# Kernel optimization log

Measured on AMD Instinct MI355X. Metric: run time of the kernel, lower is better.

## Reference

```python
import jax, jax.numpy as jnp
import numpy as np

N, E, IN_DIM, HID, L = 50000, 800000, 64, 64, 3
EDGE_DIM = 2 * HID + 2  # src_h | dst_h | edge_feat


def setup_inputs() -> dict:
    key = jax.random.key(0)
    ks = jax.random.split(key, 32)
    s = 0.05
    inp = {
        "h": jax.random.normal(ks[0], (N, IN_DIM), jnp.float32),
        "e": jax.random.normal(ks[1], (E, 2), jnp.float32),
        "src": jax.random.randint(ks[2], (E,), 0, N),
        "dst": jax.random.randint(ks[3], (E,), 0, N),
        # input embedding
        "emb_W": jax.random.normal(ks[4], (IN_DIM, HID), jnp.float32) * s,
        "emb_b": jnp.zeros((HID,), jnp.float32),
        # per-GIN-layer params (stacked over L)
        "eps": jnp.zeros((L,), jnp.float32),  # learn_eps init 0
        "mlp_W1": jax.random.normal(ks[5], (L, HID, HID), jnp.float32) * s,
        "mlp_b1": jnp.zeros((L, HID), jnp.float32),
        "mlp_bn_s": jnp.ones((L, HID), jnp.float32),   # eval-mode BN folded: x*s+sh
        "mlp_bn_sh": jnp.zeros((L, HID), jnp.float32),
        "mlp_W2": jax.random.normal(ks[6], (L, HID, HID), jnp.float32) * s,
        "mlp_b2": jnp.zeros((L, HID), jnp.float32),
        "apply_bn_s": jnp.ones((L, HID), jnp.float32),
        "apply_bn_sh": jnp.zeros((L, HID), jnp.float32),
        "gin_bn_s": jnp.ones((L, HID), jnp.float32),
        "gin_bn_sh": jnp.zeros((L, HID), jnp.float32),
        # prediction heads (L+1 of them)
        "pred_W1": jax.random.normal(ks[7], (L + 1, EDGE_DIM, HID), jnp.float32) * s,
        "pred_b1": jnp.zeros((L + 1, HID), jnp.float32),
        "pred_W2": jax.random.normal(ks[8], (L + 1, HID, 1), jnp.float32) * s,
        "pred_b2": jnp.zeros((L + 1, 1), jnp.float32),
    }
    return inp


def reference(h, e, src, dst, emb_W, emb_b, eps,
              mlp_W1, mlp_b1, mlp_bn_s, mlp_bn_sh, mlp_W2, mlp_b2,
              apply_bn_s, apply_bn_sh, gin_bn_s, gin_bn_sh,
              pred_W1, pred_b1, pred_W2, pred_b2):
    n = h.shape[0]
    bn = lambda x, sc, sh: x * sc + sh  # eval-mode batchnorm (folded scale/shift)

    h = h @ emb_W + emb_b  # [N, HID]

    def edge_feat(hh):
        # gather node features onto edges: [E, 2*HID+2]
        return jnp.concatenate([hh[src], hh[dst], e], axis=1)

    def pred(ef, i):
        z = jax.nn.relu(ef @ pred_W1[i] + pred_b1[i])
        return z @ pred_W2[i] + pred_b2[i]  # [E, 1]

    score = pred(edge_feat(h), 0)
    for i in range(L):
        h_in = h
        # GIN sum aggregation: copy src features, sum at dst
        neigh = jax.ops.segment_sum(h[src], dst, num_segments=n)
        x = (1.0 + eps[i]) * h + neigh
        # MLP: Linear -> BN -> ReLU -> Linear
        x = jax.nn.relu(bn(x @ mlp_W1[i] + mlp_b1[i], mlp_bn_s[i], mlp_bn_sh[i]))
        x = x @ mlp_W2[i] + mlp_b2[i]
        # ApplyNodeFunc: BN -> ReLU
        x = jax.nn.relu(bn(x, apply_bn_s[i], apply_bn_sh[i]))
        # GINLayer post: BN -> ReLU -> residual (dropout=0 in eval)
        x = jax.nn.relu(bn(x, gin_bn_s[i], gin_bn_sh[i]))
        h = h_in + x
        score = score + pred(edge_feat(h), i + 1)
    return jax.nn.relu(score)
```

## Files before the change

kernel.cpp:

```cpp
#include <hip/hip_runtime.h>
#include <hip/hip_bf16.h>

#define HID 64
#define L 3

typedef unsigned short ushort_t;
typedef unsigned int uint_t;

static __device__ __forceinline__ ushort_t f2bf(float f) {
    uint_t u = __float_as_uint(f);
    uint_t r = (u + 0x7FFFu + ((u >> 16) & 1u)) >> 16;
    return (ushort_t)r;
}
static __device__ __forceinline__ float bf2f(ushort_t u) {
    return __uint_as_float(((uint_t)u) << 16);
}

template <int OUT_BF16>
__global__ __launch_bounds__(256) void k_matmul16(
    const float* __restrict__ in, const float* __restrict__ W,
    const float* __restrict__ bias, void* __restrict__ out, int N)
{
    __shared__ float xs[16][68];
    const int row16 = threadIdx.x >> 4;
    const int li    = threadIdx.x & 15;
    const int r     = blockIdx.x * 16 + row16;
    if (r >= N) return;
    float4 x4 = *(const float4*)(in + (size_t)r * 64 + 4 * li);
    xs[row16][4*li+0] = x4.x; xs[row16][4*li+1] = x4.y;
    xs[row16][4*li+2] = x4.z; xs[row16][4*li+3] = x4.w;
    float4 acc;
    if (bias) acc = *(const float4*)(bias + 4 * li);
    else      acc = make_float4(0.f, 0.f, 0.f, 0.f);
#pragma unroll
    for (int k = 0; k < 64; k++) {
        float xk = xs[row16][k];
        float4 wv = *(const float4*)(W + k * 64 + 4 * li);
        acc.x += xk * wv.x; acc.y += xk * wv.y;
        acc.z += xk * wv.z; acc.w += xk * wv.w;
    }
    if (OUT_BF16) {
        ushort_t* op = (ushort_t*)out + (size_t)r * 64 + 4 * li;
        ushort4 o;
        o.x = f2bf(acc.x); o.y = f2bf(acc.y); o.z = f2bf(acc.z); o.w = f2bf(acc.w);
        *(ushort4*)op = o;
    } else {
        *(float4*)((float*)out + (size_t)r * 64 + 4 * li) = acc;
    }
}

__global__ __launch_bounds__(256) void k_gin_fused(
    const float* __restrict__ h, float* __restrict__ hout,
    const int* __restrict__ csr_src, const int* __restrict__ offsets,
    const float* __restrict__ epsp,
    const float* __restrict__ W1, const float* __restrict__ b1,
    const float* __restrict__ s1, const float* __restrict__ sh1,
    const float* __restrict__ W2, const float* __restrict__ b2,
    const float* __restrict__ as_, const float* __restrict__ ash,
    const float* __restrict__ gs, const float* __restrict__ gsh, int N)
{
    __shared__ float xs[16][68];
    __shared__ float ts[16][68];
    const int row16 = threadIdx.x >> 4;
    const int li    = threadIdx.x & 15;
    const int r     = blockIdx.x * 16 + row16;
    if (r >= N) return;

    int beg = offsets[r], end = offsets[r + 1];
    float4 acc = make_float4(0.f, 0.f, 0.f, 0.f);
    int k = beg;
    for (; k + 1 < end; k += 2) {
        int s0 = csr_src[k], s1i = csr_src[k + 1];
        float4 v0 = *(const float4*)(h + (size_t)s0 * 64 + 4 * li);
        float4 v1 = *(const float4*)(h + (size_t)s1i * 64 + 4 * li);
        acc.x += v0.x + v1.x; acc.y += v0.y + v1.y;
        acc.z += v0.z + v1.z; acc.w += v0.w + v1.w;
    }
    if (k < end) {
        int s0 = csr_src[k];
        float4 v0 = *(const float4*)(h + (size_t)s0 * 64 + 4 * li);
        acc.x += v0.x; acc.y += v0.y; acc.z += v0.z; acc.w += v0.w;
    }

    const float epsv = 1.0f + epsp[0];
    float4 hv = *(const float4*)(h + (size_t)r * 64 + 4 * li);
    xs[row16][4*li+0] = epsv * hv.x + acc.x;
    xs[row16][4*li+1] = epsv * hv.y + acc.y;
    xs[row16][4*li+2] = epsv * hv.z + acc.z;
    xs[row16][4*li+3] = epsv * hv.w + acc.w;

    float4 t = *(const float4*)(b1 + 4 * li);
#pragma unroll
    for (int kk = 0; kk < 64; kk++) {
        float xk = xs[row16][kk];
        float4 wv = *(const float4*)(W1 + kk * 64 + 4 * li);
        t.x += xk * wv.x; t.y += xk * wv.y; t.z += xk * wv.z; t.w += xk * wv.w;
    }
    {
        float4 sc = *(const float4*)(s1 + 4 * li);
        float4 sh = *(const float4*)(sh1 + 4 * li);
        t.x = t.x * sc.x + sh.x; t.x = t.x > 0.f ? t.x : 0.f;
        t.y = t.y * sc.y + sh.y; t.y = t.y > 0.f ? t.y : 0.f;
        t.z = t.z * sc.z + sh.z; t.z = t.z > 0.f ? t.z : 0.f;
        t.w = t.w * sc.w + sh.w; t.w = t.w > 0.f ? t.w : 0.f;
    }
    ts[row16][4*li+0] = t.x; ts[row16][4*li+1] = t.y;
    ts[row16][4*li+2] = t.z; ts[row16][4*li+3] = t.w;

    float4 u = *(const float4*)(b2 + 4 * li);
#pragma unroll
    for (int kk = 0; kk < 64; kk++) {
        float tk = ts[row16][kk];
        float4 wv = *(const float4*)(W2 + kk * 64 + 4 * li);
        u.x += tk * wv.x; u.y += tk * wv.y; u.z += tk * wv.z; u.w += tk * wv.w;
    }
    {
        float4 sc = *(const float4*)(as_ + 4 * li);
        float4 sh = *(const float4*)(ash + 4 * li);
        u.x = u.x * sc.x + sh.x; u.x = u.x > 0.f ? u.x : 0.f;
        u.y = u.y * sc.y + sh.y; u.y = u.y > 0.f ? u.y : 0.f;
        u.z = u.z * sc.z + sh.z; u.z = u.z > 0.f ? u.z : 0.f;
        u.w = u.w * sc.w + sh.w; u.w = u.w > 0.f ? u.w : 0.f;
        sc = *(const float4*)(gs + 4 * li);
        sh = *(const float4*)(gsh + 4 * li);
        u.x = u.x * sc.x + sh.x; u.x = u.x > 0.f ? u.x : 0.f;
        u.y = u.y * sc.y + sh.y; u.y = u.y > 0.f ? u.y : 0.f;
        u.z = u.z * sc.z + sh.z; u.z = u.z > 0.f ? u.z : 0.f;
        u.w = u.w * sc.w + sh.w; u.w = u.w > 0.f ? u.w : 0.f;
    }
    float4 o = make_float4(hv.x + u.x, hv.y + u.y, hv.z + u.z, hv.w + u.w);
    *(float4*)(hout + (size_t)r * 64 + 4 * li) = o;
}

__global__ __launch_bounds__(256) void k_count(
    const int* __restrict__ dst, int* __restrict__ deg, int E)
{
    int e = blockIdx.x * 256 + threadIdx.x;
    if (e < E) atomicAdd(&deg[dst[e]], 1);
}

__global__ __launch_bounds__(1024) void k_scan(
    int* __restrict__ cursor, int* __restrict__ offsets, int N)
{
    __shared__ int wsum[16];
    __shared__ int carry_s;
    int tid = threadIdx.x, lane = tid & 63, wid = tid >> 6;
    if (tid == 0) carry_s = 0;
    __syncthreads();
    for (int base = 0; base < N; base += 1024) {
        int idx = base + tid;
        int v = (idx < N) ? cursor[idx] : 0;
        int x = v;
#pragma unroll
        for (int o = 1; o < 64; o <<= 1) {
            int t = __shfl_up(x, o, 64);
            if (lane >= o) x += t;
        }
        if (lane == 63) wsum[wid] = x;
        __syncthreads();
        if (wid == 0) {
            int s = (lane < 16) ? wsum[lane] : 0;
#pragma unroll
            for (int o = 1; o < 16; o <<= 1) {
                int t = __shfl_up(s, o, 64);
                if (lane >= o) s += t;
            }
            if (lane < 16) wsum[lane] = s;
        }
        __syncthreads();
        int woff  = (wid > 0) ? wsum[wid - 1] : 0;
        int carry = carry_s;
        int total = wsum[15];
        int excl  = carry + woff + x - v;
        if (idx < N) { offsets[idx] = excl; cursor[idx] = excl; }
        __syncthreads();
        if (tid == 0) carry_s = carry + total;
        __syncthreads();
        if (tid == 0 && base + 1024 >= N) offsets[N] = carry + total;
    }
}

__global__ __launch_bounds__(256) void k_fill(
    const int* __restrict__ src, const int* __restrict__ dst,
    int* __restrict__ cursor, int* __restrict__ csr_src, int E)
{
    int e = blockIdx.x * 256 + threadIdx.x;
    if (e >= E) return;
    int pos = atomicAdd(&cursor[dst[e]], 1);
    csr_src[pos] = src[e];
}

template <int MODE>
__global__ __launch_bounds__(256, 4) void k_edge(
    const ushort_t* __restrict__ A, const ushort_t* __restrict__ Bm,
    const float* __restrict__ e,
    const int* __restrict__ src, const int* __restrict__ dst,
    const float* __restrict__ Wc,
    const float* __restrict__ W2,
    const float* __restrict__ b2p,
    float* __restrict__ score, int E)
{
    const int li = threadIdx.x & 15;
    const float4 wc0 = *(const float4*)(Wc + li*4);
    const float4 wc1 = *(const float4*)(Wc + 64 + li*4);
    const float4 w2  = *(const float4*)(W2 + li*4);
    const float b2 = b2p[0];
    int g  = (blockIdx.x * 256 + threadIdx.x) >> 4;
    int ng = (gridDim.x * 256) >> 4;
    for (int idx = g; idx < E; idx += ng) {
        int s = src[idx];
        int d = dst[idx];
        float2 ev = *(const float2*)(e + 2*(size_t)idx);
        ushort4 au = *(const ushort4*)(A  + (size_t)s*64 + li*4);
        ushort4 bu = *(const ushort4*)(Bm + (size_t)d*64 + li*4);
        float z0 = bf2f(au.x) + bf2f(bu.x) + ev.x*wc0.x + ev.y*wc1.x; z0 = z0 > 0.f ? z0 : 0.f;
        float z1 = bf2f(au.y) + bf2f(bu.y) + ev.x*wc0.y + ev.y*wc1.y; z1 = z1 > 0.f ? z1 : 0.f;
        float z2 = bf2f(au.z) + bf2f(bu.z) + ev.x*wc0.z + ev.y*wc1.z; z2 = z2 > 0.f ? z2 : 0.f;
        float z3 = bf2f(au.w) + bf2f(bu.w) + ev.x*wc0.w + ev.y*wc1.w; z3 = z3 > 0.f ? z3 : 0.f;
        float p = z0*w2.x + z1*w2.y + z2*w2.z + z3*w2.w;
        p += __shfl_xor(p, 1);
        p += __shfl_xor(p, 2);
        p += __shfl_xor(p, 4);
        p += __shfl_xor(p, 8);
        if (li == 0) {
            if (MODE == 0) {
                score[idx] = p + b2;
            } else if (MODE == 1) {
                score[idx] += p + b2;
            } else {
                float v = score[idx] + p + b2;
                score[idx] = v > 0.f ? v : 0.f;
            }
        }
    }
}

extern "C" void kernel_launch(void* const* d_in, const int* in_sizes, int n_in,
                              void* d_out, int out_size, void* d_ws, size_t ws_size,
                              hipStream_t stream) {
    const float* h_in  = (const float*)d_in[0];
    const float* e     = (const float*)d_in[1];
    const int*   src   = (const int*)d_in[2];
    const int*   dst   = (const int*)d_in[3];
    const float* emb_W = (const float*)d_in[4];
    const float* emb_b = (const float*)d_in[5];
    const float* eps   = (const float*)d_in[6];
    const float* mW1   = (const float*)d_in[7];
    const float* mb1   = (const float*)d_in[8];
    const float* mbs   = (const float*)d_in[9];
    const float* mbsh  = (const float*)d_in[10];
    const float* mW2   = (const float*)d_in[11];
    const float* mb2   = (const float*)d_in[12];
    const float* as_   = (const float*)d_in[13];
    const float* ash   = (const float*)d_in[14];
    const float* gs    = (const float*)d_in[15];
    const float* gsh   = (const float*)d_in[16];
    const float* pW1   = (const float*)d_in[17];
    const float* pb1   = (const float*)d_in[18];
    const float* pW2   = (const float*)d_in[19];
    const float* pb2   = (const float*)d_in[20];

    const int N = in_sizes[0] / 64;
    const int E = in_sizes[2];

    float* score = (float*)d_out;

    char* wp = (char*)d_ws;
    float* h0 = (float*)wp;         wp += (size_t)N * 64 * 4;
    float* h1 = (float*)wp;         wp += (size_t)N * 64 * 4;
    ushort_t* Abuf = (ushort_t*)wp; wp += (size_t)N * 64 * 2;
    ushort_t* Bbuf = (ushort_t*)wp; wp += (size_t)N * 64 * 2;
    int* offsets = (int*)wp;        wp += (size_t)(N + 1) * 4;
    int* cursor  = (int*)wp;        wp += (size_t)N * 4;
    int* csr_src = (int*)wp;

    const int rowBlocks = (N + 15) / 16;
    const int edgeGrid  = (E + 255) / 256;
    const int edgeBlocks = 2048;

    hipMemsetAsync(cursor, 0, (size_t)N * sizeof(int), stream);
    k_count<<<edgeGrid, 256, 0, stream>>>(dst, cursor, E);
    k_scan<<<1, 1024, 0, stream>>>(cursor, offsets, N);
    k_fill<<<edgeGrid, 256, 0, stream>>>(src, dst, cursor, csr_src, E);

    k_matmul16<0><<<rowBlocks, 256, 0, stream>>>(h_in, emb_W, emb_b, h0, N);

    float* hcur = h0;
    float* hnext = h1;

    for (int i = 0; i <= L; i++) {
        const float* pw = pW1 + (size_t)i * 130 * 64;
        k_matmul16<1><<<rowBlocks, 256, 0, stream>>>(hcur, pw,          pb1 + i*64, Abuf, N);
        k_matmul16<1><<<rowBlocks, 256, 0, stream>>>(hcur, pw + 64*64,  nullptr,    Bbuf, N);

        const float* Wc = pw + 128 * 64;
        const float* w2 = pW2 + (size_t)i * 64;
        const float* b2 = pb2 + i;
        if (i == 0) {
            k_edge<0><<<edgeBlocks, 256, 0, stream>>>(Abuf, Bbuf, e, src, dst,
                                                      Wc, w2, b2, score, E);
        } else if (i < L) {
            k_edge<1><<<edgeBlocks, 256, 0, stream>>>(Abuf, Bbuf, e, src, dst,
                                                      Wc, w2, b2, score, E);
        } else {
            k_edge<2><<<edgeBlocks, 256, 0, stream>>>(Abuf, Bbuf, e, src, dst,
                                                      Wc, w2, b2, score, E);
        }

        if (i < L) {
            k_gin_fused<<<rowBlocks, 256, 0, stream>>>(
                hcur, hnext, csr_src, offsets, eps + i,
                mW1 + (size_t)i*64*64, mb1 + i*64, mbs + i*64, mbsh + i*64,
                mW2 + (size_t)i*64*64, mb2 + i*64,
                as_ + i*64, ash + i*64, gs + i*64, gsh + i*64, N);
            float* tmp = hcur; hcur = hnext; hnext = tmp;
        }
    }
}
```

Baseline: 728.2 us.

## Fuse edge scoring into CSR-ordered GIN aggregation and merge A/B projections

Edge prediction now runs inside the per-destination GIN aggregation kernel. CSR entries carry (src, edge id), so the destination row of B is loaded once per node and the src gather for A shares the loop with aggregation. The two projection matmuls become one kernel that reads h once, and an optional bf16 copy of h halves the bytes of the neighbour gather. In exchange, score writes and edge-feature reads become scattered by edge id, work per thread follows the destination's degree, and aggregating in bf16 changes numerics.

```diff
diff --git a/kernel.cpp b/kernel.cpp
--- a/kernel.cpp
+++ b/kernel.cpp
@@ -16,10 +16,10 @@
     return __uint_as_float(((uint_t)u) << 16);
 }
 
-template <int OUT_BF16>
-__global__ __launch_bounds__(256) void k_matmul16(
+__global__ __launch_bounds__(256) void k_embed(
     const float* __restrict__ in, const float* __restrict__ W,
-    const float* __restrict__ bias, void* __restrict__ out, int N)
+    const float* __restrict__ bias, float* __restrict__ out,
+    ushort_t* __restrict__ outbf, int N)
 {
     __shared__ float xs[16][68];
     const int row16 = threadIdx.x >> 4;
@@ -29,9 +29,7 @@
     float4 x4 = *(const float4*)(in + (size_t)r * 64 + 4 * li);
     xs[row16][4*li+0] = x4.x; xs[row16][4*li+1] = x4.y;
     xs[row16][4*li+2] = x4.z; xs[row16][4*li+3] = x4.w;
-    float4 acc;
-    if (bias) acc = *(const float4*)(bias + 4 * li);
-    else      acc = make_float4(0.f, 0.f, 0.f, 0.f);
+    float4 acc = *(const float4*)(bias + 4 * li);
 #pragma unroll
     for (int k = 0; k < 64; k++) {
         float xk = xs[row16][k];
@@ -39,19 +37,113 @@
         acc.x += xk * wv.x; acc.y += xk * wv.y;
         acc.z += xk * wv.z; acc.w += xk * wv.w;
     }
-    if (OUT_BF16) {
-        ushort_t* op = (ushort_t*)out + (size_t)r * 64 + 4 * li;
+    *(float4*)(out + (size_t)r * 64 + 4 * li) = acc;
+    if (outbf) {
         ushort4 o;
         o.x = f2bf(acc.x); o.y = f2bf(acc.y); o.z = f2bf(acc.z); o.w = f2bf(acc.w);
-        *(ushort4*)op = o;
-    } else {
-        *(float4*)((float*)out + (size_t)r * 64 + 4 * li) = acc;
-    }
-}
-
-__global__ __launch_bounds__(256) void k_gin_fused(
+        *(ushort4*)(outbf + (size_t)r * 64 + 4 * li) = o;
+    }
+}
+
+__global__ __launch_bounds__(256) void k_matmulAB(
+    const float* __restrict__ h, const float* __restrict__ WA,
+    const float* __restrict__ bA, const float* __restrict__ WB,
+    ushort_t* __restrict__ A, ushort_t* __restrict__ B, int N)
+{
+    __shared__ float xs[16][68];
+    const int row16 = threadIdx.x >> 4;
+    const int li    = threadIdx.x & 15;
+    const int r     = blockIdx.x * 16 + row16;
+    if (r >= N) return;
+    float4 x4 = *(const float4*)(h + (size_t)r * 64 + 4 * li);
+    xs[row16][4*li+0] = x4.x; xs[row16][4*li+1] = x4.y;
+    xs[row16][4*li+2] = x4.z; xs[row16][4*li+3] = x4.w;
+    float4 accA = *(const float4*)(bA + 4 * li);
+    float4 accB = make_float4(0.f, 0.f, 0.f, 0.f);
+#pragma unroll
+    for (int k = 0; k < 64; k++) {
+        float xk = xs[row16][k];
+        float4 wa = *(const float4*)(WA + k * 64 + 4 * li);
+        float4 wb = *(const float4*)(WB + k * 64 + 4 * li);
+        accA.x += xk * wa.x; accA.y += xk * wa.y;
+        accA.z += xk * wa.z; accA.w += xk * wa.w;
+        accB.x += xk * wb.x; accB.y += xk * wb.y;
+        accB.z += xk * wb.z; accB.w += xk * wb.w;
+    }
+    ushort4 oa, ob;
+    oa.x = f2bf(accA.x); oa.y = f2bf(accA.y); oa.z = f2bf(accA.z); oa.w = f2bf(accA.w);
+    ob.x = f2bf(accB.x); ob.y = f2bf(accB.y); ob.z = f2bf(accB.z); ob.w = f2bf(accB.w);
+    *(ushort4*)(A + (size_t)r * 64 + 4 * li) = oa;
+    *(ushort4*)(B + (size_t)r * 64 + 4 * li) = ob;
+}
+
+__global__ __launch_bounds__(256) void k_count(
+    const int* __restrict__ dst, int* __restrict__ deg, int E)
+{
+    int e = blockIdx.x * 256 + threadIdx.x;
+    if (e < E) atomicAdd(&deg[dst[e]], 1);
+}
+
+__global__ __launch_bounds__(1024) void k_scan(
+    int* __restrict__ cursor, int* __restrict__ offsets, int N)
+{
+    __shared__ int wsum[16];
+    __shared__ int carry_s;
+    int tid = threadIdx.x, lane = tid & 63, wid = tid >> 6;
+    if (tid == 0) carry_s = 0;
+    __syncthreads();
+    for (int base = 0; base < N; base += 1024) {
+        int idx = base + tid;
+        int v = (idx < N) ? cursor[idx] : 0;
+        int x = v;
+#pragma unroll
+        for (int o = 1; o < 64; o <<= 1) {
+            int t = __shfl_up(x, o, 64);
+            if (lane >= o) x += t;
+        }
+        if (lane == 63) wsum[wid] = x;
+        __syncthreads();
+        if (wid == 0) {
+            int s = (lane < 16) ? wsum[lane] : 0;
+#pragma unroll
+            for (int o = 1; o < 16; o <<= 1) {
+                int t = __shfl_up(s, o, 64);
+                if (lane >= o) s += t;
+            }
+            if (lane < 16) wsum[lane] = s;
+        }
+        __syncthreads();
+        int woff  = (wid > 0) ? wsum[wid - 1] : 0;
+        int carry = carry_s;
+        int total = wsum[15];
+        int excl  = carry + woff + x - v;
+        if (idx < N) { offsets[idx] = excl; cursor[idx] = excl; }
+        __syncthreads();
+        if (tid == 0) carry_s = carry + total;
+        __syncthreads();
+        if (tid == 0 && base + 1024 >= N) offsets[N] = carry + total;
+    }
+}
+
+__global__ __launch_bounds__(256) void k_fill(
+    const int* __restrict__ src, const int* __restrict__ dst,
+    int* __restrict__ cursor, int2* __restrict__ csr_se, int E)
+{
+    int e = blockIdx.x * 256 + threadIdx.x;
+    if (e >= E) return;
+    int pos = atomicAdd(&cursor[dst[e]], 1);
+    csr_se[pos] = make_int2(src[e], e);
+}
+
+template <int MODE, int HASGIN, int AGGBF>
+__global__ __launch_bounds__(256) void k_fused(
     const float* __restrict__ h, float* __restrict__ hout,
-    const int* __restrict__ csr_src, const int* __restrict__ offsets,
+    const ushort_t* __restrict__ hbf, ushort_t* __restrict__ hbfout,
+    const ushort_t* __restrict__ A, const ushort_t* __restrict__ Bm,
+    const float* __restrict__ ep,
+    const int2* __restrict__ csr_se, const int* __restrict__ offsets,
+    const float* __restrict__ Wc, const float* __restrict__ W2v,
+    const float* __restrict__ b2p, float* __restrict__ score,
     const float* __restrict__ epsp,
     const float* __restrict__ W1, const float* __restrict__ b1,
     const float* __restrict__ s1, const float* __restrict__ sh1,
@@ -66,21 +158,102 @@
     const int r     = blockIdx.x * 16 + row16;
     if (r >= N) return;
 
+    const float4 wc0 = *(const float4*)(Wc + li*4);
+    const float4 wc1 = *(const float4*)(Wc + 64 + li*4);
+    const float4 w2v = *(const float4*)(W2v + li*4);
+    const float bb2 = b2p[0];
+    ushort4 bu = *(const ushort4*)(Bm + (size_t)r * 64 + li*4);
+    const float4 brow = make_float4(bf2f(bu.x), bf2f(bu.y), bf2f(bu.z), bf2f(bu.w));
+
     int beg = offsets[r], end = offsets[r + 1];
     float4 acc = make_float4(0.f, 0.f, 0.f, 0.f);
+
     int k = beg;
     for (; k + 1 < end; k += 2) {
-        int s0 = csr_src[k], s1i = csr_src[k + 1];
-        float4 v0 = *(const float4*)(h + (size_t)s0 * 64 + 4 * li);
-        float4 v1 = *(const float4*)(h + (size_t)s1i * 64 + 4 * li);
-        acc.x += v0.x + v1.x; acc.y += v0.y + v1.y;
-        acc.z += v0.z + v1.z; acc.w += v0.w + v1.w;
+        int2 se0 = csr_se[k];
+        int2 se1 = csr_se[k + 1];
+        ushort4 a0 = *(const ushort4*)(A + (size_t)se0.x * 64 + li*4);
+        ushort4 a1 = *(const ushort4*)(A + (size_t)se1.x * 64 + li*4);
+        float2 ev0 = *(const float2*)(ep + 2*(size_t)se0.y);
+        float2 ev1 = *(const float2*)(ep + 2*(size_t)se1.y);
+        if (HASGIN) {
+            if (AGGBF) {
+                ushort4 h0 = *(const ushort4*)(hbf + (size_t)se0.x * 64 + li*4);
+                ushort4 h1 = *(const ushort4*)(hbf + (size_t)se1.x * 64 + li*4);
+                acc.x += bf2f(h0.x) + bf2f(h1.x);
+                acc.y += bf2f(h0.y) + bf2f(h1.y);
+                acc.z += bf2f(h0.z) + bf2f(h1.z);
+                acc.w += bf2f(h0.w) + bf2f(h1.w);
+            } else {
+                float4 h0 = *(const float4*)(h + (size_t)se0.x * 64 + li*4);
+                float4 h1 = *(const float4*)(h + (size_t)se1.x * 64 + li*4);
+                acc.x += h0.x + h1.x; acc.y += h0.y + h1.y;
+                acc.z += h0.z + h1.z; acc.w += h0.w + h1.w;
+            }
+        }
+        float z0 = bf2f(a0.x) + brow.x + ev0.x*wc0.x + ev0.y*wc1.x; z0 = z0 > 0.f ? z0 : 0.f;
+        float z1 = bf2f(a0.y) + brow.y + ev0.x*wc0.y + ev0.y*wc1.y; z1 = z1 > 0.f ? z1 : 0.f;
+        float z2 = bf2f(a0.z) + brow.z + ev0.x*wc0.z + ev0.y*wc1.z; z2 = z2 > 0.f ? z2 : 0.f;
+        float z3 = bf2f(a0.w) + brow.w + ev0.x*wc0.w + ev0.y*wc1.w; z3 = z3 > 0.f ? z3 : 0.f;
+        float p0 = z0*w2v.x + z1*w2v.y + z2*w2v.z + z3*w2v.w;
+        z0 = bf2f(a1.x) + brow.x + ev1.x*wc0.x + ev1.y*wc1.x; z0 = z0 > 0.f ? z0 : 0.f;
+        z1 = bf2f(a1.y) + brow.y + ev1.x*wc0.y + ev1.y*wc1.y; z1 = z1 > 0.f ? z1 : 0.f;
+        z2 = bf2f(a1.z) + brow.z + ev1.x*wc0.z + ev1.y*wc1.z; z2 = z2 > 0.f ? z2 : 0.f;
+        z3 = bf2f(a1.w) + brow.w + ev1.x*wc0.w + ev1.y*wc1.w; z3 = z3 > 0.f ? z3 : 0.f;
+        float p1 = z0*w2v.x + z1*w2v.y + z2*w2v.z + z3*w2v.w;
+        p0 += __shfl_xor(p0, 1); p1 += __shfl_xor(p1, 1);
+        p0 += __shfl_xor(p0, 2); p1 += __shfl_xor(p1, 2);
+        p0 += __shfl_xor(p0, 4); p1 += __shfl_xor(p1, 4);
+        p0 += __shfl_xor(p0, 8); p1 += __shfl_xor(p1, 8);
+        if (li == 0) {
+            if (MODE == 0) {
+                score[se0.y] = p0 + bb2;
+                score[se1.y] = p1 + bb2;
+            } else if (MODE == 1) {
+                score[se0.y] += p0 + bb2;
+                score[se1.y] += p1 + bb2;
+            } else {
+                float v0 = score[se0.y] + p0 + bb2;
+                float v1 = score[se1.y] + p1 + bb2;
+                score[se0.y] = v0 > 0.f ? v0 : 0.f;
+                score[se1.y] = v1 > 0.f ? v1 : 0.f;
+            }
+        }
     }
     if (k < end) {
-        int s0 = csr_src[k];
-        float4 v0 = *(const float4*)(h + (size_t)s0 * 64 + 4 * li);
-        acc.x += v0.x; acc.y += v0.y; acc.z += v0.z; acc.w += v0.w;
-    }
+        int2 se0 = csr_se[k];
+        ushort4 a0 = *(const ushort4*)(A + (size_t)se0.x * 64 + li*4);
+        float2 ev0 = *(const float2*)(ep + 2*(size_t)se0.y);
+        if (HASGIN) {
+            if (AGGBF) {
+                ushort4 h0 = *(const ushort4*)(hbf + (size_t)se0.x * 64 + li*4);
+                acc.x += bf2f(h0.x); acc.y += bf2f(h0.y);
+                acc.z += bf2f(h0.z); acc.w += bf2f(h0.w);
+            } else {
+                float4 h0 = *(const float4*)(h + (size_t)se0.x * 64 + li*4);
+                acc.x += h0.x; acc.y += h0.y; acc.z += h0.z; acc.w += h0.w;
+            }
+        }
+        float z0 = bf2f(a0.x) + brow.x + ev0.x*wc0.x + ev0.y*wc1.x; z0 = z0 > 0.f ? z0 : 0.f;
+        float z1 = bf2f(a0.y) + brow.y + ev0.x*wc0.y + ev0.y*wc1.y; z1 = z1 > 0.f ? z1 : 0.f;
+        float z2 = bf2f(a0.z) + brow.z + ev0.x*wc0.z + ev0.y*wc1.z; z2 = z2 > 0.f ? z2 : 0.f;
+        float z3 = bf2f(a0.w) + brow.w + ev0.x*wc0.w + ev0.y*wc1.w; z3 = z3 > 0.f ? z3 : 0.f;
+        float p0 = z0*w2v.x + z1*w2v.y + z2*w2v.z + z3*w2v.w;
+        p0 += __shfl_xor(p0, 1);
+        p0 += __shfl_xor(p0, 2);
+        p0 += __shfl_xor(p0, 4);
+        p0 += __shfl_xor(p0, 8);
+        if (li == 0) {
+            if (MODE == 0)      score[se0.y] = p0 + bb2;
+            else if (MODE == 1) score[se0.y] += p0 + bb2;
+            else {
+                float v0 = score[se0.y] + p0 + bb2;
+                score[se0.y] = v0 > 0.f ? v0 : 0.f;
+            }
+        }
+    }
+
+    if (!HASGIN) return;
 
     const float epsv = 1.0f + epsp[0];
     float4 hv = *(const float4*)(h + (size_t)r * 64 + 4 * li);
@@ -130,108 +303,10 @@
     }
     float4 o = make_float4(hv.x + u.x, hv.y + u.y, hv.z + u.z, hv.w + u.w);
     *(float4*)(hout + (size_t)r * 64 + 4 * li) = o;
-}
-
-__global__ __launch_bounds__(256) void k_count(
-    const int* __restrict__ dst, int* __restrict__ deg, int E)
-{
-    int e = blockIdx.x * 256 + threadIdx.x;
-    if (e < E) atomicAdd(&deg[dst[e]], 1);
-}
-
-__global__ __launch_bounds__(1024) void k_scan(
-    int* __restrict__ cursor, int* __restrict__ offsets, int N)
-{
-    __shared__ int wsum[16];
-    __shared__ int carry_s;
-    int tid = threadIdx.x, lane = tid & 63, wid = tid >> 6;
-    if (tid == 0) carry_s = 0;
-    __syncthreads();
-    for (int base = 0; base < N; base += 1024) {
-        int idx = base + tid;
-        int v = (idx < N) ? cursor[idx] : 0;
-        int x = v;
-#pragma unroll
-        for (int o = 1; o < 64; o <<= 1) {
-            int t = __shfl_up(x, o, 64);
-            if (lane >= o) x += t;
-        }
-        if (lane == 63) wsum[wid] = x;
-        __syncthreads();
-        if (wid == 0) {
-            int s = (lane < 16) ? wsum[lane] : 0;
-#pragma unroll
-            for (int o = 1; o < 16; o <<= 1) {
-                int t = __shfl_up(s, o, 64);
-                if (lane >= o) s += t;
-            }
-            if (lane < 16) wsum[lane] = s;
-        }
-        __syncthreads();
-        int woff  = (wid > 0) ? wsum[wid - 1] : 0;
-        int carry = carry_s;
-        int total = wsum[15];
-        int excl  = carry + woff + x - v;
-        if (idx < N) { offsets[idx] = excl; cursor[idx] = excl; }
-        __syncthreads();
-        if (tid == 0) carry_s = carry + total;
-        __syncthreads();
-        if (tid == 0 && base + 1024 >= N) offsets[N] = carry + total;
-    }
-}
-
-__global__ __launch_bounds__(256) void k_fill(
-    const int* __restrict__ src, const int* __restrict__ dst,
-    int* __restrict__ cursor, int* __restrict__ csr_src, int E)
-{
-    int e = blockIdx.x * 256 + threadIdx.x;
-    if (e >= E) return;
-    int pos = atomicAdd(&cursor[dst[e]], 1);
-    csr_src[pos] = src[e];
-}
-
-template <int MODE>
-__global__ __launch_bounds__(256, 4) void k_edge(
-    const ushort_t* __restrict__ A, const ushort_t* __restrict__ Bm,
-    const float* __restrict__ e,
-    const int* __restrict__ src, const int* __restrict__ dst,
-    const float* __restrict__ Wc,
-    const float* __restrict__ W2,
-    const float* __restrict__ b2p,
-    float* __restrict__ score, int E)
-{
-    const int li = threadIdx.x & 15;
-    const float4 wc0 = *(const float4*)(Wc + li*4);
-    const float4 wc1 = *(const float4*)(Wc + 64 + li*4);
-    const float4 w2  = *(const float4*)(W2 + li*4);
-    const float b2 = b2p[0];
-    int g  = (blockIdx.x * 256 + threadIdx.x) >> 4;
-    int ng = (gridDim.x * 256) >> 4;
-    for (int idx = g; idx < E; idx += ng) {
-        int s = src[idx];
-        int d = dst[idx];
-        float2 ev = *(const float2*)(e + 2*(size_t)idx);
-        ushort4 au = *(const ushort4*)(A  + (size_t)s*64 + li*4);
-        ushort4 bu = *(const ushort4*)(Bm + (size_t)d*64 + li*4);
-        float z0 = bf2f(au.x) + bf2f(bu.x) + ev.x*wc0.x + ev.y*wc1.x; z0 = z0 > 0.f ? z0 : 0.f;
-        float z1 = bf2f(au.y) + bf2f(bu.y) + ev.x*wc0.y + ev.y*wc1.y; z1 = z1 > 0.f ? z1 : 0.f;
-        float z2 = bf2f(au.z) + bf2f(bu.z) + ev.x*wc0.z + ev.y*wc1.z; z2 = z2 > 0.f ? z2 : 0.f;
-        float z3 = bf2f(au.w) + bf2f(bu.w) + ev.x*wc0.w + ev.y*wc1.w; z3 = z3 > 0.f ? z3 : 0.f;
-        float p = z0*w2.x + z1*w2.y + z2*w2.z + z3*w2.w;
-        p += __shfl_xor(p, 1);
-        p += __shfl_xor(p, 2);
-        p += __shfl_xor(p, 4);
-        p += __shfl_xor(p, 8);
-        if (li == 0) {
-            if (MODE == 0) {
-                score[idx] = p + b2;
-            } else if (MODE == 1) {
-                score[idx] += p + b2;
-            } else {
-                float v = score[idx] + p + b2;
-                score[idx] = v > 0.f ? v : 0.f;
-            }
-        }
+    if (AGGBF) {
+        ushort4 ob;
+        ob.x = f2bf(o.x); ob.y = f2bf(o.y); ob.z = f2bf(o.z); ob.w = f2bf(o.w);
+        *(ushort4*)(hbfout + (size_t)r * 64 + 4 * li) = ob;
     }
 }
 
@@ -262,58 +337,82 @@
 
     const int N = in_sizes[0] / 64;
     const int E = in_sizes[2];
+    const size_t nrow = (size_t)N * 64;
 
     float* score = (float*)d_out;
 
     char* wp = (char*)d_ws;
-    float* h0 = (float*)wp;         wp += (size_t)N * 64 * 4;
-    float* h1 = (float*)wp;         wp += (size_t)N * 64 * 4;
-    ushort_t* Abuf = (ushort_t*)wp; wp += (size_t)N * 64 * 2;
-    ushort_t* Bbuf = (ushort_t*)wp; wp += (size_t)N * 64 * 2;
-    int* offsets = (int*)wp;        wp += (size_t)(N + 1) * 4;
-    int* cursor  = (int*)wp;        wp += (size_t)N * 4;
-    int* csr_src = (int*)wp;
+    float* h0 = (float*)wp;          wp += nrow * 4;
+    float* h1 = (float*)wp;          wp += nrow * 4;
+    ushort_t* Abuf = (ushort_t*)wp;  wp += nrow * 2;
+    ushort_t* Bbuf = (ushort_t*)wp;  wp += nrow * 2;
+    int2* csr_se = (int2*)wp;        wp += (size_t)E * 8;
+    int* offsets = (int*)wp;         wp += (size_t)(N + 1) * 4;
+    int* cursor  = (int*)wp;         wp += (size_t)N * 4;
+    size_t base_need = (size_t)(wp - (char*)d_ws);
+    ushort_t* hbf0 = (ushort_t*)wp;
+    ushort_t* hbf1 = (ushort_t*)(wp + nrow * 2);
+    const bool use_bf = ws_size >= base_need + 2 * nrow * 2;
+    if (!use_bf) { hbf0 = nullptr; hbf1 = nullptr; }
 
     const int rowBlocks = (N + 15) / 16;
     const int edgeGrid  = (E + 255) / 256;
-    const int edgeBlocks = 2048;
 
     hipMemsetAsync(cursor, 0, (size_t)N * sizeof(int), stream);
     k_count<<<edgeGrid, 256, 0, stream>>>(dst, cursor, E);
     k_scan<<<1, 1024, 0, stream>>>(cursor, offsets, N);
-    k_fill<<<edgeGrid, 256, 0, stream>>>(src, dst, cursor, csr_src, E);
-
-    k_matmul16<0><<<rowBlocks, 256, 0, stream>>>(h_in, emb_W, emb_b, h0, N);
-
-    float* hcur = h0;
-    float* hnext = h1;
+    k_fill<<<edgeGrid, 256, 0, stream>>>(src, dst, cursor, csr_se, E);
+
+    k_embed<<<rowBlocks, 256, 0, stream>>>(h_in, emb_W, emb_b, h0, hbf0, N);
+
+    float* hcur = h0;     float* hnext = h1;
+    ushort_t* bcur = hbf0; ushort_t* bnext = hbf1;
 
     for (int i = 0; i <= L; i++) {
         const float* pw = pW1 + (size_t)i * 130 * 64;
-        k_matmul16<1><<<rowBlocks, 256, 0, stream>>>(hcur, pw,          pb1 + i*64, Abuf, N);
-        k_matmul16<1><<<rowBlocks, 256, 0, stream>>>(hcur, pw + 64*64,  nullptr,    Bbuf, N);
-
+        k_matmulAB<<<rowBlocks, 256, 0, stream>>>(hcur, pw, pb1 + i*64, pw + 64*64,
+                                                  Abuf, Bbuf, N);
         const float* Wc = pw + 128 * 64;
         const float* w2 = pW2 + (size_t)i * 64;
         const float* b2 = pb2 + i;
-        if (i == 0) {
-            k_edge<0><<<edgeBlocks, 256, 0, stream>>>(Abuf, Bbuf, e, src, dst,
-                                                      Wc, w2, b2, score, E);
-        } else if (i < L) {
-            k_edge<1><<<edgeBlocks, 256, 0, stream>>>(Abuf, Bbuf, e, src, dst,
-                                                      Wc, w2, b2, score, E);
+
+        if (i < L) {
+            const float* gW1 = mW1 + (size_t)i*64*64;
+            const float* gW2 = mW2 + (size_t)i*64*64;
+            if (use_bf) {
+                if (i == 0)
+                    k_fused<0,1,1><<<rowBlocks, 256, 0, stream>>>(
+                        hcur, hnext, bcur, bnext, Abuf, Bbuf, e, csr_se, offsets,
+                        Wc, w2, b2, score, eps + i, gW1, mb1 + i*64, mbs + i*64,
+                        mbsh + i*64, gW2, mb2 + i*64, as_ + i*64, ash + i*64,
+                        gs + i*64, gsh + i*64, N);
+                else
+                    k_fused<1,1,1><<<rowBlocks, 256, 0, stream>>>(
+                        hcur, hnext, bcur, bnext, Abuf, Bbuf, e, csr_se, offsets,
+                        Wc, w2, b2, score, eps + i, gW1, mb1 + i*64, mbs + i*64,
+                        mbsh + i*64, gW2, mb2 + i*64, as_ + i*64, ash + i*64,
+                        gs + i*64, gsh + i*64, N);
+            } else {
+                if (i == 0)
+                    k_fused<0,1,0><<<rowBlocks, 256, 0, stream>>>(
+                        hcur, hnext, bcur, bnext, Abuf, Bbuf, e, csr_se, offsets,
+                        Wc, w2, b2, score, eps + i, gW1, mb1 + i*64, mbs + i*64,
+                        mbsh + i*64, gW2, mb2 + i*64, as_ + i*64, ash + i*64,
+                        gs + i*64, gsh + i*64, N);
+                else
+                    k_fused<1,1,0><<<rowBlocks, 256, 0, stream>>>(
+                        hcur, hnext, bcur, bnext, Abuf, Bbuf, e, csr_se, offsets,
+                        Wc, w2, b2, score, eps + i, gW1, mb1 + i*64, mbs + i*64,
+                        mbsh + i*64, gW2, mb2 + i*64, as_ + i*64, ash + i*64,
+                        gs + i*64, gsh + i*64, N);
+            }
+            { float* t = hcur; hcur = hnext; hnext = t; }
+            { ushort_t* t = bcur; bcur = bnext; bnext = t; }
         } else {
-            k_edge<2><<<edgeBlocks, 256, 0, stream>>>(Abuf, Bbuf, e, src, dst,
-                                                      Wc, w2, b2, score, E);
-        }
-
-        if (i < L) {
-            k_gin_fused<<<rowBlocks, 256, 0, stream>>>(
-                hcur, hnext, csr_src, offsets, eps + i,
-                mW1 + (size_t)i*64*64, mb1 + i*64, mbs + i*64, mbsh + i*64,
-                mW2 + (size_t)i*64*64, mb2 + i*64,
-                as_ + i*64, ash + i*64, gs + i*64, gsh + i*64, N);
-            float* tmp = hcur; hcur = hnext; hnext = tmp;
-        }
-    }
-}
+            k_fused<2,0,0><<<rowBlocks, 256, 0, stream>>>(
+                hcur, nullptr, nullptr, nullptr, Abuf, Bbuf, e, csr_se, offsets,
+                Wc, w2, b2, score, nullptr, nullptr, nullptr, nullptr,
+                nullptr, nullptr, nullptr, nullptr, nullptr, nullptr, nullptr, N);
+        }
+    }
+}
```

After: 808.5 us. 1.11x slower.
